# Performance work log

Hardware: AMD Instinct MI355X
Metric: run time of the kernel (lower is better)

## Reference

```python
import jax, jax.numpy as jnp
import numpy as np
import math

EMBED_DIM = 768
NUM_HEADS = 12
HEAD_DIM = EMBED_DIM // NUM_HEADS
EPS = 1e-6


def setup_inputs() -> dict:
    key = jax.random.key(0)
    ks = jax.random.split(key, 9)
    T, B, N, D = 4, 4, 1024, EMBED_DIM
    s = 0.02
    return {
        "x": jax.random.normal(ks[0], (T, B, N, D), dtype=jnp.float32),
        "Wq": jax.random.normal(ks[1], (D, D), dtype=jnp.float32) * s,
        "bq": jax.random.normal(ks[2], (D,), dtype=jnp.float32) * s,
        "Wk": jax.random.normal(ks[3], (D, D), dtype=jnp.float32) * s,
        "bk": jax.random.normal(ks[4], (D,), dtype=jnp.float32) * s,
        "Wv": jax.random.normal(ks[5], (D, D), dtype=jnp.float32) * s,
        "bv": jax.random.normal(ks[6], (D,), dtype=jnp.float32) * s,
        "Wo": jax.random.normal(ks[7], (D, D), dtype=jnp.float32) * s,
        "bo": jax.random.normal(ks[8], (D,), dtype=jnp.float32) * s,
    }


def _split_heads(y, T, B, N):
    # [T,B,N,D] -> [T,B,H,N,Dh]
    return y.reshape(T, B, N, NUM_HEADS, HEAD_DIM).transpose(0, 1, 3, 2, 4)


def reference(x, Wq, bq, Wk, bk, Wv, bv, Wo, bo):
    T, B, N, D = x.shape
    # q/k/v projections (nn.Linear: x @ W^T + b)
    q = _split_heads(x @ Wq.T + bq, T, B, N)
    k = _split_heads(x @ Wk.T + bk, T, B, N)
    v = _split_heads(x @ Wv.T + bv, T, B, N)
    # scores = q k^T / sqrt(head_dim)
    scores = jnp.einsum("tbhnd,tbhmd->tbhnm", q, k) / math.sqrt(HEAD_DIM)
    # spike-form normalization: relu then L1-normalize along keys
    act = jax.nn.relu(scores)
    attn = act / (act.sum(axis=-1, keepdims=True) + EPS)
    ctx = jnp.einsum("tbhnm,tbhmd->tbhnd", attn, v)
    # merge heads: [T,B,H,N,Dh] -> [T,B,N,D]
    out = ctx.transpose(0, 1, 3, 2, 4).reshape(T, B, N, D)
    return out @ Wo.T + bo
```

## Files before the change

### kernel.cpp

```cpp
#include <hip/hip_runtime.h>
#include <hip/hip_bf16.h>
#include <cstdint>


typedef __attribute__((ext_vector_type(8))) short short8;
typedef __attribute__((ext_vector_type(4))) float float4v;
typedef __attribute__((ext_vector_type(16))) float float16v;

__device__ __forceinline__ unsigned short f2bf(float f) {
  unsigned int u = __float_as_uint(f);
  u = (u + 0x7fffu + ((u >> 16) & 1u)) >> 16;
  return (unsigned short)u;
}

__device__ __forceinline__ unsigned int pkbf(float a, float b) {
  unsigned int ua = __float_as_uint(a) + 0x8000u;
  unsigned int ub = __float_as_uint(b) + 0x8000u;
  return __builtin_amdgcn_perm(ub, ua, 0x07060302u);
}

__device__ __forceinline__ void gld_lds16(const void* g, void* lds) {
  __builtin_amdgcn_global_load_lds(
      (__attribute__((address_space(1))) void*)(uintptr_t)g,
      (__attribute__((address_space(3))) void*)(uint32_t)(uintptr_t)lds,
      16, 0, 0);
}

__global__ __launch_bounds__(256) void cast_all(
    const float* __restrict__ x,  const float* __restrict__ Wq,
    const float* __restrict__ Wk, const float* __restrict__ Wv,
    const float* __restrict__ Wo, unsigned short* __restrict__ XBF,
    unsigned short* __restrict__ WQKV, unsigned short* __restrict__ WOb) {
  const int bid = blockIdx.x;
  const float* src;
  unsigned short* dst;
  int i;
  if (bid < 12288) {
    src = x; dst = XBF; i = bid * 256 + threadIdx.x;
  } else {
    const int wb = bid - 12288;
    const int which = wb / 576;
    i = (wb % 576) * 256 + threadIdx.x;
    src = (which == 0) ? Wq : (which == 1) ? Wk : (which == 2) ? Wv : Wo;
    dst = (which == 0) ? WQKV
        : (which == 1) ? WQKV + 589824
        : (which == 2) ? WQKV + 1179648 : WOb;
  }
  float4 f = reinterpret_cast<const float4*>(src)[i];
  ushort4 o;
  o.x = f2bf(f.x); o.y = f2bf(f.y); o.z = f2bf(f.z); o.w = f2bf(f.w);
  reinterpret_cast<ushort4*>(dst)[i] = o;
}

template <bool OUT_BF16>
__global__ __launch_bounds__(256) void gemm_bt(
    const unsigned short* __restrict__ A,
    const unsigned short* __restrict__ Bt,
    unsigned short* __restrict__ Cb,
    float* __restrict__ Cf,
    unsigned short* __restrict__ Vt,
    const float* __restrict__ b0, const float* __restrict__ b1,
    const float* __restrict__ b2, int N) {
  constexpr int K = 768;
  __shared__ unsigned short As[128 * 32];
  __shared__ unsigned short Bs[128 * 32];

  const int tid = threadIdx.x;
  const int lane = tid & 63;
  const int w = tid >> 6;
  const int wrow = w >> 1, wcol = w & 1;
  const int l15 = lane & 15, quad = lane >> 4;
  const int i0 = blockIdx.y * 128, j0 = blockIdx.x * 128;

  const unsigned short* ga = A + (size_t)(i0 + 32 * w + (lane >> 2)) * K + (lane & 3) * 8;
  const unsigned short* gb = Bt + (size_t)(j0 + 32 * w + (lane >> 2)) * K + (lane & 3) * 8;

  float4v acc[4][4];
#pragma unroll
  for (int a = 0; a < 4; ++a)
#pragma unroll
    for (int b = 0; b < 4; ++b) acc[a][b] = float4v{0.f, 0.f, 0.f, 0.f};

#pragma unroll 1
  for (int kt = 0; kt < K / 32; ++kt) {
    const unsigned short* pa = ga + kt * 32;
    const unsigned short* pb = gb + kt * 32;
    gld_lds16(pa, &As[(32 * w) * 32]);
    gld_lds16(pa + 16 * K, &As[(32 * w + 16) * 32]);
    gld_lds16(pb, &Bs[(32 * w) * 32]);
    gld_lds16(pb + 16 * K, &Bs[(32 * w + 16) * 32]);
    __syncthreads();

    short8 af[4], bfr[4];
#pragma unroll
    for (int a = 0; a < 4; ++a)
      af[a] = *(const short8*)&As[(wrow * 64 + a * 16 + l15) * 32 + quad * 8];
#pragma unroll
    for (int b = 0; b < 4; ++b)
      bfr[b] = *(const short8*)&Bs[(wcol * 64 + b * 16 + l15) * 32 + quad * 8];
#pragma unroll
    for (int a = 0; a < 4; ++a)
#pragma unroll
      for (int b = 0; b < 4; ++b)
        acc[a][b] = __builtin_amdgcn_mfma_f32_16x16x32_bf16(af[a], bfr[b], acc[a][b], 0, 0, 0);
    __syncthreads();
  }

  const int sel = j0 / 768;
  const float* bp = (sel == 0) ? b0 : ((sel == 1) ? b1 : b2);
#pragma unroll
  for (int a = 0; a < 4; ++a) {
    const int row0 = i0 + wrow * 64 + a * 16 + quad * 4;
#pragma unroll
    for (int b = 0; b < 4; ++b) {
      const int col = j0 + wcol * 64 + b * 16 + l15;
      const float bias = bp[col - sel * 768];
      if (OUT_BF16 && sel == 2) {
        const int tb = row0 >> 10;
        const int n0 = row0 & 1023;
        const int hd = col - 1536;
        const float v0 = acc[a][b][0] + bias;
        const float v1 = acc[a][b][1] + bias;
        const float v2 = acc[a][b][2] + bias;
        const float v3 = acc[a][b][3] + bias;
        uint2 u;
        u.x = (unsigned int)f2bf(v0) | ((unsigned int)f2bf(v1) << 16);
        u.y = (unsigned int)f2bf(v2) | ((unsigned int)f2bf(v3) << 16);
        *(uint2*)&Vt[((size_t)(tb * 768 + hd)) * 1024 + n0] = u;
      } else {
#pragma unroll
        for (int r = 0; r < 4; ++r) {
          const float v = acc[a][b][r] + bias;
          if (OUT_BF16)
            Cb[(size_t)(row0 + r) * N + col] = f2bf(v);
          else
            Cf[(size_t)(row0 + r) * N + col] = v;
        }
      }
    }
  }
}

__global__ __launch_bounds__(256) void attn32(
    const unsigned short* __restrict__ qkv,
    const unsigned short* __restrict__ vt,
    unsigned short* __restrict__ ctx) {
  __shared__ unsigned short Ks[64 * 72];
  __shared__ unsigned short Vs[64 * 72];

  const int tbh = blockIdx.x;
  const int qt = blockIdx.y;
  const int tb = tbh / 12, h = tbh % 12;
  const int tid = threadIdx.x, lane = tid & 63, w = tid >> 6;
  const int l31 = lane & 31, hl = lane >> 5;

  short8 qf[2][4];
#pragma unroll
  for (int qs = 0; qs < 2; ++qs) {
    const unsigned short* qp =
        qkv + (size_t)(tb * 1024 + qt * 256 + w * 64 + qs * 32 + l31) * 2304 +
        h * 64 + hl * 8;
#pragma unroll
    for (int kc = 0; kc < 4; ++kc) qf[qs][kc] = *(const short8*)(qp + kc * 16);
  }

  const int srow = tid >> 3;
  const int sblk = tid & 7;
  const unsigned short* kcol =
      qkv + (size_t)(tb * 1024) * 2304 + 768 + h * 64 + sblk * 8;
  const unsigned short* vcol = vt + ((size_t)tbh * 64 + srow) * 1024 + sblk * 8;
  uint4 kr0, kr1, vr0, vr1;
  auto loadKV = [&](int kv) {
    const unsigned short* kp = kcol + (size_t)(kv * 64 + srow) * 2304;
    kr0 = *(const uint4*)kp;
    kr1 = *(const uint4*)(kp + 32 * 2304);
    const unsigned short* vp = vcol + kv * 64;
    vr0 = *(const uint4*)vp;
    vr1 = *(const uint4*)(vp + 32 * 1024);
  };

  float16v octx[2][2];
#pragma unroll
  for (int qs = 0; qs < 2; ++qs)
#pragma unroll
    for (int dt = 0; dt < 2; ++dt)
#pragma unroll
      for (int i = 0; i < 16; ++i) octx[qs][dt][i] = 0.f;
  float den[2] = {0.f, 0.f};

  loadKV(0);

#pragma unroll 1
  for (int kv = 0; kv < 16; ++kv) {
    __syncthreads();
    *(uint4*)&Ks[srow * 72 + sblk * 8] = kr0;
    *(uint4*)&Ks[(srow + 32) * 72 + sblk * 8] = kr1;
    *(uint4*)&Vs[srow * 72 + sblk * 8] = vr0;
    *(uint4*)&Vs[(srow + 32) * 72 + sblk * 8] = vr1;
    __syncthreads();
    if (kv < 15) loadKV(kv + 1);

#pragma unroll
    for (int qs = 0; qs < 2; ++qs) {
      unsigned int pk[2][8];
#pragma unroll
      for (int mt = 0; mt < 2; ++mt) {
        float16v st;
#pragma unroll
        for (int i = 0; i < 16; ++i) st[i] = 0.f;
#pragma unroll
        for (int kc = 0; kc < 4; ++kc) {
          short8 kf =
              *(const short8*)&Ks[(mt * 32 + l31) * 72 + kc * 16 + hl * 8];
          st = __builtin_amdgcn_mfma_f32_32x32x16_bf16(kf, qf[qs][kc], st, 0, 0, 0);
        }
#pragma unroll
        for (int g = 0; g < 4; ++g) {
          float v0 = st[4 * g + 0]; v0 = v0 > 0.f ? v0 : 0.f;
          float v1 = st[4 * g + 1]; v1 = v1 > 0.f ? v1 : 0.f;
          float v2 = st[4 * g + 2]; v2 = v2 > 0.f ? v2 : 0.f;
          float v3 = st[4 * g + 3]; v3 = v3 > 0.f ? v3 : 0.f;
          den[qs] += (v0 + v1) + (v2 + v3);
          pk[mt][g * 2 + 0] = pkbf(v0, v1);
          pk[mt][g * 2 + 1] = pkbf(v2, v3);
        }
      }
#pragma unroll
      for (int kc = 0; kc < 4; ++kc) {
        const int mt = kc >> 1, gb = (kc & 1) * 2;
        unsigned int a0 = pk[mt][gb * 2 + 0], b0 = pk[mt][gb * 2 + 2];
        unsigned int a1 = pk[mt][gb * 2 + 1], b1 = pk[mt][gb * 2 + 3];
        asm("v_permlane32_swap_b32 %0, %1" : "+v"(a0), "+v"(b0));
        asm("v_permlane32_swap_b32 %0, %1" : "+v"(a1), "+v"(b1));
        union { unsigned int u[4]; short8 s; } pf;
        pf.u[0] = a0; pf.u[1] = a1; pf.u[2] = b0; pf.u[3] = b1;
#pragma unroll
        for (int dt = 0; dt < 2; ++dt) {
          short8 vb =
              *(const short8*)&Vs[(dt * 32 + l31) * 72 + kc * 16 + hl * 8];
          octx[qs][dt] = __builtin_amdgcn_mfma_f32_32x32x16_bf16(
              vb, pf.s, octx[qs][dt], 0, 0, 0);
        }
      }
    }
  }

#pragma unroll
  for (int qs = 0; qs < 2; ++qs) {
    float d = den[qs] + __shfl_xor(den[qs], 32);
    const float sc = 1.f / (d + 8e-6f);
    const size_t qrow = (size_t)(tb * 1024 + qt * 256 + w * 64 + qs * 32 + l31);
#pragma unroll
    for (int dt = 0; dt < 2; ++dt)
#pragma unroll
      for (int g = 0; g < 4; ++g) {
        const float v0 = octx[qs][dt][4 * g + 0] * sc;
        const float v1 = octx[qs][dt][4 * g + 1] * sc;
        const float v2 = octx[qs][dt][4 * g + 2] * sc;
        const float v3 = octx[qs][dt][4 * g + 3] * sc;
        uint2 u;
        u.x = pkbf(v0, v1);
        u.y = pkbf(v2, v3);
        *(uint2*)&ctx[qrow * 768 + h * 64 + dt * 32 + g * 8 + hl * 4] = u;
      }
  }
}

extern "C" void kernel_launch(void* const* d_in, const int* in_sizes, int n_in,
                              void* d_out, int out_size, void* d_ws, size_t ws_size,
                              hipStream_t stream) {
  const float* x  = (const float*)d_in[0];
  const float* Wq = (const float*)d_in[1];
  const float* bq = (const float*)d_in[2];
  const float* Wk = (const float*)d_in[3];
  const float* bk = (const float*)d_in[4];
  const float* Wv = (const float*)d_in[5];
  const float* bv = (const float*)d_in[6];
  const float* Wo = (const float*)d_in[7];
  const float* bo = (const float*)d_in[8];
  float* out = (float*)d_out;

  char* ws = (char*)d_ws;
  unsigned short* XBF  = (unsigned short*)(ws);
  unsigned short* CTX  = (unsigned short*)(ws);
  unsigned short* WQKV = (unsigned short*)(ws + 25165824);
  unsigned short* WOb  = (unsigned short*)(ws + 28704768);
  unsigned short* QKV  = (unsigned short*)(ws + 29884416);
  unsigned short* VT   = (unsigned short*)(ws + 105381888);

  cast_all<<<14592, 256, 0, stream>>>(x, Wq, Wk, Wv, Wo, XBF, WQKV, WOb);

  gemm_bt<true><<<dim3(18, 128), 256, 0, stream>>>(XBF, WQKV, QKV, nullptr, VT,
                                                   bq, bk, bv, 2304);
  attn32<<<dim3(192, 4), 256, 0, stream>>>(QKV, VT, CTX);
  gemm_bt<false><<<dim3(6, 128), 256, 0, stream>>>(CTX, WOb, nullptr, out,
                                                   nullptr, bo, bo, bo, 768);
}
```

Baseline: 343.7 us.

## Double-buffer GEMM LDS tiles and remap workgroups across XCDs

The bf16 GEMM now uses two LDS buffers per operand. The next K-tile is issued with global_load_lds while the MFMAs run on the current tile, so load latency can overlap compute. Workgroup IDs are also remapped in groups of eight, apparently so that tiles sharing A/B rows land on the same XCD's L2. The cost is double the LDS footprint (32KB), which may reduce occupancy. The remap assumes the workgroup count divides by 8, and correctness depends on the single remaining barrier per iteration ordering buffer reuse properly.

Result: faster. 316.4 us (-8.0%).

```diff
diff --git a/kernel.cpp b/kernel.cpp
--- a/kernel.cpp
+++ b/kernel.cpp
@@ -62,15 +62,22 @@
     const float* __restrict__ b0, const float* __restrict__ b1,
     const float* __restrict__ b2, int N) {
   constexpr int K = 768;
-  __shared__ unsigned short As[128 * 32];
-  __shared__ unsigned short Bs[128 * 32];
+  __shared__ unsigned short As[2][128 * 32];
+  __shared__ unsigned short Bs[2][128 * 32];
 
   const int tid = threadIdx.x;
   const int lane = tid & 63;
   const int w = tid >> 6;
   const int wrow = w >> 1, wcol = w & 1;
   const int l15 = lane & 15, quad = lane >> 4;
-  const int i0 = blockIdx.y * 128, j0 = blockIdx.x * 128;
+
+  const int gx = gridDim.x;
+  const int nwg = gx * gridDim.y;
+  const int hw = blockIdx.y * gx + blockIdx.x;
+  const int per = nwg >> 3;
+  const int lg = (hw & 7) * per + (hw >> 3);
+  const int bx = lg % gx, by = lg / gx;
+  const int i0 = by * 128, j0 = bx * 128;
 
   const unsigned short* ga = A + (size_t)(i0 + 32 * w + (lane >> 2)) * K + (lane & 3) * 8;
   const unsigned short* gb = Bt + (size_t)(j0 + 32 * w + (lane >> 2)) * K + (lane & 3) * 8;
@@ -81,23 +88,31 @@
 #pragma unroll
     for (int b = 0; b < 4; ++b) acc[a][b] = float4v{0.f, 0.f, 0.f, 0.f};
 
+  gld_lds16(ga, &As[0][(32 * w) * 32]);
+  gld_lds16(ga + 16 * K, &As[0][(32 * w + 16) * 32]);
+  gld_lds16(gb, &Bs[0][(32 * w) * 32]);
+  gld_lds16(gb + 16 * K, &Bs[0][(32 * w + 16) * 32]);
+  __syncthreads();
+
 #pragma unroll 1
   for (int kt = 0; kt < K / 32; ++kt) {
-    const unsigned short* pa = ga + kt * 32;
-    const unsigned short* pb = gb + kt * 32;
-    gld_lds16(pa, &As[(32 * w) * 32]);
-    gld_lds16(pa + 16 * K, &As[(32 * w + 16) * 32]);
-    gld_lds16(pb, &Bs[(32 * w) * 32]);
-    gld_lds16(pb + 16 * K, &Bs[(32 * w + 16) * 32]);
-    __syncthreads();
+    const int cur = kt & 1;
+    if (kt < K / 32 - 1) {
+      const unsigned short* pa = ga + (kt + 1) * 32;
+      const unsigned short* pb = gb + (kt + 1) * 32;
+      gld_lds16(pa, &As[cur ^ 1][(32 * w) * 32]);
+      gld_lds16(pa + 16 * K, &As[cur ^ 1][(32 * w + 16) * 32]);
+      gld_lds16(pb, &Bs[cur ^ 1][(32 * w) * 32]);
+      gld_lds16(pb + 16 * K, &Bs[cur ^ 1][(32 * w + 16) * 32]);
+    }
 
     short8 af[4], bfr[4];
 #pragma unroll
     for (int a = 0; a < 4; ++a)
-      af[a] = *(const short8*)&As[(wrow * 64 + a * 16 + l15) * 32 + quad * 8];
+      af[a] = *(const short8*)&As[cur][(wrow * 64 + a * 16 + l15) * 32 + quad * 8];
 #pragma unroll
     for (int b = 0; b < 4; ++b)
-      bfr[b] = *(const short8*)&Bs[(wcol * 64 + b * 16 + l15) * 32 + quad * 8];
+      bfr[b] = *(const short8*)&Bs[cur][(wcol * 64 + b * 16 + l15) * 32 + quad * 8];
 #pragma unroll
     for (int a = 0; a < 4; ++a)
 #pragma unroll
```
